# Kernel tuning notes

Measured on AMD Instinct MI355X. Metric: run time of the kernel, lower is better.

## Reference

```python
import jax, jax.numpy as jnp
import numpy as np

EMBEDDING_DIM = 256
SCALE_STEP = 2
NUM_SCALES = EMBEDDING_DIM // 4  # 64


def setup_inputs() -> dict:
    key = jax.random.key(0)
    B = 500000
    # lat/lon in degrees (roughly earth-like ranges via scaled normal)
    lat_lon_deg = jax.random.normal(key, (B, 2), dtype=jnp.float32) * 45.0
    return {"lat_lon_deg": lat_lon_deg}


def reference(lat_lon_deg):
    B = lat_lon_deg.shape[0]
    rad = jnp.deg2rad(lat_lon_deg)                       # [B, 2]
    scales = (SCALE_STEP ** jnp.arange(NUM_SCALES)).astype(rad.dtype)  # [S]
    lat = rad[:, 0:1] * scales                           # [B, S]
    lon = rad[:, 1:2] * scales                           # [B, S]
    # per scale layout: [sin(lat), cos(lat), sin(lon), cos(lon)]
    feats = jnp.stack(
        [jnp.sin(lat), jnp.cos(lat), jnp.sin(lon), jnp.cos(lon)], axis=-1
    )                                                    # [B, S, 4]
    features = feats.reshape(B, 1, NUM_SCALES * 4)       # [B, 1, 256]
    mask = jnp.zeros((B, 1), dtype=bool)
    positions = jnp.zeros((B, 1, 1, 2), dtype=features.dtype)
    return features, mask, positions
```

## Files before the change

### kernel.cpp

```cpp
#include <hip/hip_runtime.h>


typedef float f32x4 __attribute__((ext_vector_type(4)));

__global__ __launch_bounds__(256) void posfeat_kernel(const float* __restrict__ ll,
                                                      f32x4* __restrict__ out,
                                                      int B, long long n4) {
    const double QHI = 0x1.45F306DC9C883p-3;
    const float DEG2RAD = 0.017453292519943295f;

    const long long featUnits = (long long)B * 64;
    const long long stride = (long long)gridDim.x * 256;
    const long long tid0 = (long long)blockIdx.x * 256 + threadIdx.x;
    const f32x4 ZERO4 = {0.f, 0.f, 0.f, 0.f};

    for (long long u = tid0; u < featUnits; u += stride) {
        int b = (int)(u >> 6);
        int s = (int)(u & 63);
        float2 p = reinterpret_cast<const float2*>(ll)[b];
        float rlat = p.x * DEG2RAD;
        float rlon = p.y * DEG2RAD;
        double ya = (double)rlat * QHI;
        double yb = (double)rlon * QHI;
        double va = ldexp(ya, s);
        double vb = ldexp(yb, s);
        if (s == 31) { va = -va; vb = -vb; }
        double fa = va - floor(va);
        double fb = vb - floor(vb);
        float ra = (float)fa, rb = (float)fb;
        f32x4 o;
        o.x = __builtin_amdgcn_sinf(ra);
        o.y = __builtin_amdgcn_cosf(ra);
        o.z = __builtin_amdgcn_sinf(rb);
        o.w = __builtin_amdgcn_cosf(rb);
        if (s >= 32) { o.x = 0.f; o.y = 1.f; o.z = 0.f; o.w = 1.f; }
        __builtin_nontemporal_store(o, &out[u]);
    }

    for (long long z = featUnits + tid0; z < n4; z += stride) {
        __builtin_nontemporal_store(ZERO4, &out[z]);
    }
}

__global__ void tail_zero_kernel(float* __restrict__ z, int n) {
    int t = threadIdx.x;
    if (t < n) z[t] = 0.f;
}

extern "C" void kernel_launch(void* const* d_in, const int* in_sizes, int n_in,
                              void* d_out, int out_size, void* d_ws, size_t ws_size,
                              hipStream_t stream) {
    const float* ll = (const float*)d_in[0];
    float* out = (float*)d_out;
    int B = in_sizes[0] / 2;

    long long n4 = (long long)out_size >> 2;
    posfeat_kernel<<<8192, 256, 0, stream>>>(ll, (f32x4*)out, B, n4);

    int tail = out_size & 3;
    if (tail) {
        tail_zero_kernel<<<1, 64, 0, stream>>>(out + ((long long)out_size - tail), tail);
    }
}
```

Measured before the change: 113.2 us.

## Assign points per block with shared staging and dedicated zero-fill blocks

Replaces the grid-stride loop with a fixed mapping of 64 points per block. One warp loads and converts each point's lat/lon into shared memory, and all threads then compute the 64 scales from it. Separate leading blocks handle the zero-fill of the mask and positions region. The aim is to remove redundant per-unit input loads and 64-bit index math, at the cost of a __syncthreads and a much larger grid.

Result: faster. 108.0 us (-4.6%).

```diff
diff --git a/kernel.cpp b/kernel.cpp
--- a/kernel.cpp
+++ b/kernel.cpp
@@ -2,43 +2,62 @@
 
 
 typedef float f32x4 __attribute__((ext_vector_type(4)));
+
+#define PTS_PER_BLOCK 64
+#define ZERO_BLOCKS   128
 
 __global__ __launch_bounds__(256) void posfeat_kernel(const float* __restrict__ ll,
                                                       f32x4* __restrict__ out,
                                                       int B, long long n4) {
     const double QHI = 0x1.45F306DC9C883p-3;
     const float DEG2RAD = 0.017453292519943295f;
+    const long long featUnits = (long long)B * 64;
 
-    const long long featUnits = (long long)B * 64;
-    const long long stride = (long long)gridDim.x * 256;
-    const long long tid0 = (long long)blockIdx.x * 256 + threadIdx.x;
-    const f32x4 ZERO4 = {0.f, 0.f, 0.f, 0.f};
+    if (blockIdx.x < ZERO_BLOCKS) {
+        const f32x4 ZERO4 = {0.f, 0.f, 0.f, 0.f};
+        const long long stride = (long long)ZERO_BLOCKS * 256;
+        for (long long z = featUnits + (long long)blockIdx.x * 256 + threadIdx.x;
+             z < n4; z += stride)
+            __builtin_nontemporal_store(ZERO4, &out[z]);
+        return;
+    }
 
-    for (long long u = tid0; u < featUnits; u += stride) {
-        int b = (int)(u >> 6);
-        int s = (int)(u & 63);
-        float2 p = reinterpret_cast<const float2*>(ll)[b];
+    __shared__ double yll[PTS_PER_BLOCK][2];
+    const int fb = blockIdx.x - ZERO_BLOCKS;
+    const int p0 = fb * PTS_PER_BLOCK;
+    const int t = threadIdx.x;
+
+    if (t < PTS_PER_BLOCK) {
+        int b = p0 + t;
+        float2 p = (b < B) ? reinterpret_cast<const float2*>(ll)[b]
+                           : make_float2(0.f, 0.f);
         float rlat = p.x * DEG2RAD;
         float rlon = p.y * DEG2RAD;
-        double ya = (double)rlat * QHI;
-        double yb = (double)rlon * QHI;
-        double va = ldexp(ya, s);
-        double vb = ldexp(yb, s);
+        yll[t][0] = (double)rlat * QHI;
+        yll[t][1] = (double)rlon * QHI;
+    }
+    __syncthreads();
+
+    const long long ubase = (long long)p0 * 64;
+    const int s = t & 63;
+    #pragma unroll
+    for (int i = 0; i < (PTS_PER_BLOCK * 64) / 256; ++i) {
+        int idx = i * 256 + t;
+        long long u = ubase + idx;
+        if (u >= featUnits) break;
+        int pl = idx >> 6;
+        double ya = yll[pl][0], yb = yll[pl][1];
+        double va = ldexp(ya, s), vb = ldexp(yb, s);
         if (s == 31) { va = -va; vb = -vb; }
-        double fa = va - floor(va);
-        double fb = vb - floor(vb);
-        float ra = (float)fa, rb = (float)fb;
+        double fa = va - floor(va), fb2 = vb - floor(vb);
+        float ra = (float)fa, rb = (float)fb2;
         f32x4 o;
         o.x = __builtin_amdgcn_sinf(ra);
         o.y = __builtin_amdgcn_cosf(ra);
         o.z = __builtin_amdgcn_sinf(rb);
         o.w = __builtin_amdgcn_cosf(rb);
-        if (s >= 32) { o.x = 0.f; o.y = 1.f; o.z = 0.f; o.w = 1.f; }
+        if (s >= 32) { o = (f32x4){0.f, 1.f, 0.f, 1.f}; }
         __builtin_nontemporal_store(o, &out[u]);
-    }
-
-    for (long long z = featUnits + tid0; z < n4; z += stride) {
-        __builtin_nontemporal_store(ZERO4, &out[z]);
     }
 }
 
@@ -55,7 +74,8 @@
     int B = in_sizes[0] / 2;
 
     long long n4 = (long long)out_size >> 2;
-    posfeat_kernel<<<8192, 256, 0, stream>>>(ll, (f32x4*)out, B, n4);
+    int featBlocks = (B + PTS_PER_BLOCK - 1) / PTS_PER_BLOCK;
+    posfeat_kernel<<<featBlocks + ZERO_BLOCKS, 256, 0, stream>>>(ll, (f32x4*)out, B, n4);
 
     int tail = out_size & 3;
     if (tail) {
```
